# Optimization experiments

Hardware: AMD Instinct MI355X
Metric: run time of the kernel (lower is better)

The kernel has to match this reference:

```python
import jax, jax.numpy as jnp
import numpy as np

AABB0 = np.array([-1.5, -1.5, -1.5], np.float32)
AABB1 = np.array([1.5, 1.5, 1.5], np.float32)
GRID = (300, 300, 300)
NEAR, FAR = 2.0, 6.0
STEP = float(np.mean((AABB1 - AABB0) / (np.array(GRID, np.float32) - 1)) * 0.5)  # step_ratio=0.5
DIST_SCALE = 25.0
DENSITY_SHIFT = -10.0
W_THRES = 1e-4
PE = 2  # view_pe = feat_pe = 2
MAT = ((0, 1), (0, 2), (1, 2))
VEC = (2, 1, 0)
N_RAYS, N_SAMP = 1024, 512
DN, AN = 16, 16
APP_DIM, FEAT_C = 27, 128
IN_MLP = 2 * PE * 3 + 2 * PE * APP_DIM + 3 + APP_DIM  # 150


def posenc(x, freqs):
    fb = (2.0 ** jnp.arange(freqs)).astype(x.dtype)
    p = (x[..., None] * fb).reshape(x.shape[:-1] + (x.shape[-1] * freqs,))
    return jnp.concatenate([jnp.sin(p), jnp.cos(p)], -1)


def bilinear2d(plane, xy):
    # plane [C,H,W]; xy [P,2] in [-1,1], x->W, y->H; align_corners=True, border clamp
    C, H, W = plane.shape
    x = jnp.clip((xy[:, 0] * 0.5 + 0.5) * (W - 1), 0.0, W - 1)
    y = jnp.clip((xy[:, 1] * 0.5 + 0.5) * (H - 1), 0.0, H - 1)
    x0 = jnp.clip(jnp.floor(x), 0, W - 2).astype(jnp.int32)
    y0 = jnp.clip(jnp.floor(y), 0, H - 2).astype(jnp.int32)
    wx, wy = x - x0, y - y0
    v00 = plane[:, y0, x0]
    v01 = plane[:, y0, x0 + 1]
    v10 = plane[:, y0 + 1, x0]
    v11 = plane[:, y0 + 1, x0 + 1]
    return (v00 * (1 - wx) + v01 * wx) * (1 - wy) + (v10 * (1 - wx) + v11 * wx) * wy  # [C,P]


def linear1d(line, z):
    # line [C,L]; z [P] in [-1,1]
    C, L = line.shape
    t = jnp.clip((z * 0.5 + 0.5) * (L - 1), 0.0, L - 1)
    i0 = jnp.clip(jnp.floor(t), 0, L - 2).astype(jnp.int32)
    w = t - i0
    return line[:, i0] * (1 - w) + line[:, i0 + 1] * w  # [C,P]


def _forward(rays_o, rays_d, dplanes, dlines, aplanes, alines, basis_w,
             w1, b1, w2, b2, w3, b3, n_samples):
    a0, a1 = jnp.asarray(AABB0), jnp.asarray(AABB1)
    # --- sample_ray (is_train=False) ---
    vec = jnp.where(rays_d == 0, 1e-6, rays_d)
    rate_a = (a1 - rays_o) / vec
    rate_b = (a0 - rays_o) / vec
    t_min = jnp.clip(jnp.max(jnp.minimum(rate_a, rate_b), -1), NEAR, FAR)  # [R]
    rng = jnp.arange(n_samples, dtype=rays_o.dtype)[None]
    z_vals = t_min[:, None] + STEP * rng  # [R,S]
    pts = rays_o[:, None, :] + rays_d[:, None, :] * z_vals[..., None]  # [R,S,3]
    ray_valid = jnp.all((pts >= a0) & (pts <= a1), -1)  # [R,S]
    xn = ((pts - a0) * (2.0 / (a1 - a0)) - 1.0).reshape(-1, 3)  # normalize_coord -> [P,3]
    # --- density: VM decomposition (sum of plane*line products) ---
    sigma_feat = jnp.zeros((xn.shape[0],), xn.dtype)
    for i in range(3):
        p = bilinear2d(dplanes[i], xn[:, jnp.array(MAT[i])])
        l = linear1d(dlines[i], xn[:, VEC[i]])
        sigma_feat = sigma_feat + jnp.sum(p * l, 0)
    sigma = jax.nn.softplus(sigma_feat + DENSITY_SHIFT).reshape(z_vals.shape)
    sigma = jnp.where(ray_valid, sigma, 0.0)
    # --- raw2alpha compositing ---
    dists = jnp.concatenate([z_vals[:, 1:] - z_vals[:, :-1], jnp.zeros_like(z_vals[:, :1])], -1)
    alpha = 1.0 - jnp.exp(-sigma * dists * DIST_SCALE)
    T = jnp.cumprod(jnp.concatenate([jnp.ones_like(alpha[:, :1]), 1.0 - alpha + 1e-10], -1), -1)
    weight = alpha * T[:, :-1]
    app_mask = weight > W_THRES
    # --- appearance features + basis_mat ---
    coefs = [bilinear2d(aplanes[i], xn[:, jnp.array(MAT[i])]) * linear1d(alines[i], xn[:, VEC[i]])
             for i in range(3)]
    feat = jnp.concatenate(coefs, 0).T @ basis_w.T  # [P, app_dim]
    view = jnp.broadcast_to(rays_d[:, None, :], pts.shape).reshape(-1, 3)
    # --- MLPRender_Fea: [features, viewdirs, posenc(features), posenc(viewdirs)] ---
    mlp_in = jnp.concatenate([feat, view, posenc(feat, PE), posenc(view, PE)], -1)
    h = jax.nn.relu(mlp_in @ w1.T + b1)
    h = jax.nn.relu(h @ w2.T + b2)
    rgb = jax.nn.sigmoid(h @ w3.T + b3).reshape(z_vals.shape + (3,))
    rgb = jnp.where(app_mask[..., None], rgb, 0.0)
    acc = jnp.sum(weight, -1)
    rgb_map = jnp.sum(weight[..., None] * rgb, 1)
    rgb_map = jnp.clip(rgb_map + (1.0 - acc)[:, None], 0.0, 1.0)  # white background
    depth_map = jnp.sum(weight * z_vals, -1)
    return rgb_map, depth_map


def setup_inputs() -> dict:
    key = jax.random.key(0)
    ks = jax.random.split(key, 20)
    rd = jax.random.normal(ks[0], (N_RAYS, 3), jnp.float32)
    rays_d = rd / jnp.linalg.norm(rd, axis=-1, keepdims=True)
    rays_o = -3.0 * rays_d + 0.1 * jax.random.normal(ks[1], (N_RAYS, 3), jnp.float32)
    inp = {"rays_o": rays_o, "rays_d": rays_d}
    for i, ((m0, m1), v) in enumerate(zip(MAT, VEC)):
        inp[f"dplane{i}"] = jax.random.normal(ks[2 + i], (DN, GRID[m1], GRID[m0]), jnp.float32)
        inp[f"dline{i}"] = jax.random.normal(ks[5 + i], (DN, GRID[v]), jnp.float32)
        inp[f"aplane{i}"] = 0.1 * jax.random.normal(ks[8 + i], (AN, GRID[m1], GRID[m0]), jnp.float32)
        inp[f"aline{i}"] = 0.1 * jax.random.normal(ks[11 + i], (AN, GRID[v]), jnp.float32)
    inp["basis_w"] = 0.1 * jax.random.normal(ks[14], (APP_DIM, 3 * AN), jnp.float32)
    inp["w1"] = 0.05 * jax.random.normal(ks[15], (FEAT_C, IN_MLP), jnp.float32)
    inp["b1"] = jnp.zeros((FEAT_C,), jnp.float32)
    inp["w2"] = 0.05 * jax.random.normal(ks[16], (FEAT_C, FEAT_C), jnp.float32)
    inp["b2"] = jnp.zeros((FEAT_C,), jnp.float32)
    inp["w3"] = 0.05 * jax.random.normal(ks[17], (3, FEAT_C), jnp.float32)
    inp["b3"] = jnp.zeros((3,), jnp.float32)
    inp["n_samples"] = N_SAMP
    return inp


def reference(rays_o, rays_d, dplane0, dplane1, dplane2, dline0, dline1, dline2,
              aplane0, aplane1, aplane2, aline0, aline1, aline2, basis_w,
              w1, b1, w2, b2, w3, b3, n_samples):
    return _forward(rays_o, rays_d, (dplane0, dplane1, dplane2), (dline0, dline1, dline2),
                    (aplane0, aplane1, aplane2), (aline0, aline1, aline2), basis_w,
                    w1, b1, w2, b2, w3, b3, n_samples)
```

## Files before the change

kernel.cpp:

```cpp
#include <hip/hip_runtime.h>
#include <hip/hip_fp16.h>
#include <math.h>

#define NRAYS 1024
#define NSAMP 512
#define GRIDN 300
#define POS_ELEMS (GRIDN*GRIDN)
#define PLANE_ELEMS (16*POS_ELEMS)
#define CMAX 524288

typedef short bf16x8 __attribute__((ext_vector_type(8)));
typedef short short8 __attribute__((ext_vector_type(8)));
typedef float f32x4  __attribute__((ext_vector_type(4)));

struct H8v { __half2 h[4]; };

__device__ __forceinline__ float clampf(float x, float a, float b){ return fminf(fmaxf(x,a),b); }
__device__ __forceinline__ unsigned short f2b(float f){
    unsigned u = __builtin_bit_cast(unsigned, f);
    u = (u + 0x7FFFu + ((u>>16)&1u)) >> 16;
    return (unsigned short)u;
}
__device__ __forceinline__ float b2f(unsigned short h){
    unsigned u = ((unsigned)h) << 16;
    return __builtin_bit_cast(float, u);
}

__device__ __forceinline__ float ray_tmin(float o0,float o1,float o2,float d0,float d1,float d2){
    float v0=(d0==0.f)?1e-6f:d0, v1=(d1==0.f)?1e-6f:d1, v2=(d2==0.f)?1e-6f:d2;
    float t_min = -1e30f, a, b;
    a=(1.5f-o0)/v0; b=(-1.5f-o0)/v0; t_min=fmaxf(t_min,fminf(a,b));
    a=(1.5f-o1)/v1; b=(-1.5f-o1)/v1; t_min=fmaxf(t_min,fminf(a,b));
    a=(1.5f-o2)/v2; b=(-1.5f-o2)/v2; t_min=fmaxf(t_min,fminf(a,b));
    return clampf(t_min, 2.0f, 6.0f);
}

struct TPtrs {
    const float* psrc[6]; __half* pdst[6];
    const float* lsrc[6]; __half* ldst[6];
};

__global__ __launch_bounds__(256) void k_transpose(TPtrs tp) {
    int by  = blockIdx.y;
    int pos = blockIdx.x * 256 + threadIdx.x;
    if (pos < POS_ELEMS) {
        const float* src = tp.psrc[by];
        __half2 o[8];
        #pragma unroll
        for (int e = 0; e < 8; e++) {
            float a = src[(2*e  ) * POS_ELEMS + pos];
            float b = src[(2*e+1) * POS_ELEMS + pos];
            o[e] = __float22half2_rn(make_float2(a,b));
        }
        float4* dst = (float4*)(tp.pdst[by] + (size_t)pos * 16);
        dst[0] = *(float4*)&o[0];
        dst[1] = *(float4*)&o[4];
    }
    if (pos < GRIDN) {
        const float* ls = tp.lsrc[by];
        __half*      ld = tp.ldst[by];
        #pragma unroll
        for (int c = 0; c < 16; c++) ld[pos * 16 + c] = __float2half_rn(ls[c * GRIDN + pos]);
    }
}

__global__ __launch_bounds__(256) void k_prepw(
    const float* __restrict__ w1, const float* __restrict__ w2,
    unsigned short* __restrict__ w1b, unsigned short* __restrict__ w2b)
{
    int idx = blockIdx.x * 256 + threadIdx.x;
    if (idx < 128*160) {
        int j = idx / 160, k = idx - j*160;
        w1b[idx] = (k < 150) ? f2b(w1[j*150 + k]) : 0;
    } else if (idx < 128*160 + 128*128) {
        int i2 = idx - 128*160;
        w2b[i2] = f2b(w2[i2]);
    }
}

__global__ __launch_bounds__(256) void k_alpha(
    const float* __restrict__ ro, const float* __restrict__ rd,
    const __half* __restrict__ dpT0, const __half* __restrict__ dpT1, const __half* __restrict__ dpT2,
    const __half* __restrict__ dlT0, const __half* __restrict__ dlT1, const __half* __restrict__ dlT2,
    float* __restrict__ alpha_out)
{
    const float STEPF = (3.0f/299.0f)*0.5f;
    int gid = blockIdx.x*256 + threadIdx.x;
    int id = gid >> 1, h = gid & 1;
    int r = id >> 9, s = id & (NSAMP-1);

    float o0=ro[r*3+0], o1=ro[r*3+1], o2=ro[r*3+2];
    float d0=rd[r*3+0], d1=rd[r*3+1], d2=rd[r*3+2];
    float t_min = ray_tmin(o0,o1,o2,d0,d1,d2);

    float z  = t_min + STEPF * (float)s;
    float p0 = o0 + d0*z, p1 = o1 + d1*z, p2 = o2 + d2*z;
    bool valid = (p0>=-1.5f)&&(p0<=1.5f)&&(p1>=-1.5f)&&(p1<=1.5f)&&(p2>=-1.5f)&&(p2<=1.5f);

    float sfp = 0.f;
    if (valid) {
        float xn[3] = { (p0+1.5f)*(2.0f/3.0f)-1.0f,
                        (p1+1.5f)*(2.0f/3.0f)-1.0f,
                        (p2+1.5f)*(2.0f/3.0f)-1.0f };
        const __half* dpT[3] = {dpT0,dpT1,dpT2};
        const __half* dlT[3] = {dlT0,dlT1,dlT2};
        const int M0[3]={0,0,1}, M1[3]={1,2,2}, V[3]={2,1,0};
        #pragma unroll
        for (int i=0;i<3;i++) {
            float fx = clampf((xn[M0[i]]*0.5f+0.5f)*299.f, 0.f, 299.f);
            float fy = clampf((xn[M1[i]]*0.5f+0.5f)*299.f, 0.f, 299.f);
            float ft = clampf((xn[V[i]] *0.5f+0.5f)*299.f, 0.f, 299.f);
            int x0=min((int)fx,298), y0=min((int)fy,298), i0=min((int)ft,298);
            float wx=fx-(float)x0, wy=fy-(float)y0, wt=ft-(float)i0;
            __half2 w00=__float2half2_rn((1.f-wx)*(1.f-wy)), w01=__float2half2_rn(wx*(1.f-wy));
            __half2 w10=__float2half2_rn((1.f-wx)*wy),       w11=__float2half2_rn(wx*wy);
            __half2 u0 =__float2half2_rn(1.f-wt),            u1 =__float2half2_rn(wt);
            const __half* base = dpT[i] + (size_t)(y0*GRIDN+x0)*16 + h*8;
            H8v a00 = *(const H8v*)(base);
            H8v a01 = *(const H8v*)(base + 16);
            H8v a10 = *(const H8v*)(base + GRIDN*16);
            H8v a11 = *(const H8v*)(base + GRIDN*16 + 16);
            const __half* lb = dlT[i] + (size_t)i0*16 + h*8;
            H8v l0 = *(const H8v*)(lb);
            H8v l1 = *(const H8v*)(lb + 16);
            #pragma unroll
            for (int e=0;e<4;e++) {
                __half2 p = __hmul2(a00.h[e],w00);
                p = __hfma2(a01.h[e],w01,p);
                p = __hfma2(a10.h[e],w10,p);
                p = __hfma2(a11.h[e],w11,p);
                __half2 l = __hmul2(l0.h[e],u0);
                l = __hfma2(l1.h[e],u1,l);
                float2 c = __half22float2(__hmul2(p,l));
                sfp += c.x + c.y;
            }
        }
    }
    float sf = sfp + __shfl_xor(sfp, 1, 64);
    if (h == 0) {
        float sig = 0.f;
        if (valid) {
            float xs = sf - 10.0f;
            sig = fmaxf(xs, 0.f) + __logf(1.f + __expf(-fabsf(xs)));
        }
        alpha_out[id] = (s < NSAMP-1) ? (1.f - __expf(-sig * (STEPF*25.0f))) : 0.f;
    }
}

__global__ __launch_bounds__(256) void k_scan(
    const float* __restrict__ ro, const float* __restrict__ rd,
    const float* __restrict__ alpha_in,
    float* __restrict__ acc_out, float* __restrict__ depth_out,
    int* __restrict__ tmpl, float* __restrict__ tmpw, int* __restrict__ cnt)
{
    const float STEPF = (3.0f/299.0f)*0.5f;
    int r = blockIdx.x;
    int tid = threadIdx.x;
    int lane = tid & 63, wv = tid >> 6;

    float o0=ro[r*3+0], o1=ro[r*3+1], o2=ro[r*3+2];
    float d0=rd[r*3+0], d1=rd[r*3+1], d2=rd[r*3+2];
    float t_min = ray_tmin(o0,o1,o2,d0,d1,d2);

    float2 av = *(const float2*)&alpha_in[r*NSAMP + 2*tid];
    float aj0 = av.x, aj1 = av.y;
    float zj0 = t_min + STEPF * (float)(2*tid);
    float zj1 = t_min + STEPF * (float)(2*tid+1);

    float v0 = (1.f - aj0) + 1e-10f;
    float v1 = (1.f - aj1) + 1e-10f;
    float inc = v0 * v1;
    #pragma unroll
    for (int off=1; off<64; off<<=1) {
        float t = __shfl_up(inc, off, 64);
        if (lane >= off) inc *= t;
    }
    __shared__ float wtot[4], swsum[4], sdep[4];
    __shared__ int   wcnt[4];
    if (lane == 63) wtot[wv] = inc;
    __syncthreads();
    float pre = 1.f;
    for (int i=0;i<wv;i++) pre *= wtot[i];
    float excl = __shfl_up(inc, 1, 64);
    if (lane == 0) excl = 1.f;
    float T0 = pre * excl;
    float w0 = aj0 * T0;
    float w1 = aj1 * T0 * v0;

    float rw = w0 + w1, rz = w0*zj0 + w1*zj1;
    #pragma unroll
    for (int off=32; off>0; off>>=1) { rw += __shfl_xor(rw,off,64); rz += __shfl_xor(rz,off,64); }
    if (lane == 0) { swsum[wv] = rw; sdep[wv] = rz; }

    bool act0 = (w0 > 1e-4f), act1 = (w1 > 1e-4f);
    unsigned long long m0 = __ballot(act0);
    unsigned long long m1 = __ballot(act1);
    int tot = __popcll(m0) + __popcll(m1);
    if (lane == 0) wcnt[wv] = tot;
    __syncthreads();
    int base = 0;
    for (int i=0;i<wv;i++) base += wcnt[i];
    unsigned long long below = (1ull<<lane)-1ull;
    int o = base + __popcll(m0 & below) + __popcll(m1 & below);
    int* tl = tmpl + r*NSAMP;
    float* tw = tmpw + r*NSAMP;
    if (act0) { tl[o] = (r<<9)|(2*tid);   tw[o] = w0; o++; }
    if (act1) { tl[o] = (r<<9)|(2*tid+1); tw[o] = w1; }

    if (tid == 0) {
        float a=0.f, b=0.f;
        #pragma unroll
        for (int i=0;i<4;i++){ a+=swsum[i]; b+=sdep[i]; }
        acc_out[r] = a; depth_out[r] = b;
        cnt[r] = wcnt[0]+wcnt[1]+wcnt[2]+wcnt[3];
    }
}

__global__ __launch_bounds__(256) void k_compact(
    const int* __restrict__ tmpl, const float* __restrict__ tmpw,
    const int* __restrict__ cnt,
    int* __restrict__ basep, int* __restrict__ counter,
    int* __restrict__ list, float* __restrict__ wlist)
{
    int r = blockIdx.x;
    int tid = threadIdx.x, lane = tid & 63, wv = tid >> 6;

    int accb = 0, acct = 0;
    for (int i = tid; i < NRAYS; i += 256) {
        int c = cnt[i];
        acct += c;
        if (i < r) accb += c;
    }
    #pragma unroll
    for (int off=32; off>0; off>>=1) {
        accb += __shfl_xor(accb, off, 64);
        acct += __shfl_xor(acct, off, 64);
    }
    __shared__ int sb[4], st[4];
    if (lane == 0) { sb[wv] = accb; st[wv] = acct; }
    __syncthreads();
    int b = sb[0]+sb[1]+sb[2]+sb[3];
    int n = cnt[r];
    if (tid == 0) {
        basep[r] = b;
        if (r == 0) *counter = st[0]+st[1]+st[2]+st[3];
    }
    const int* tl = tmpl + r*NSAMP;
    const float* tw = tmpw + r*NSAMP;
    for (int j = tid; j < n; j += 256) {
        list[b+j]  = tl[j];
        wlist[b+j] = tw[j];
    }
}

__global__ __launch_bounds__(256) void k_gather(
    const float* __restrict__ ro, const float* __restrict__ rd,
    const __half* __restrict__ apT0, const __half* __restrict__ apT1, const __half* __restrict__ apT2,
    const __half* __restrict__ alT0, const __half* __restrict__ alT1, const __half* __restrict__ alT2,
    const float* __restrict__ basis_w,
    const int* __restrict__ list, const int* __restrict__ counter,
    float* __restrict__ Xf)
{
    const float STEPF = (3.0f/299.0f)*0.5f;
    int gid = blockIdx.x*256 + threadIdx.x;
    int idx = gid >> 3, q = gid & 7;
    int count = *counter;
    if (idx >= count) return;

    int sid = list[idx];
    int r = sid >> 9, s = sid & (NSAMP-1);
    float o0=ro[r*3+0], o1=ro[r*3+1], o2=ro[r*3+2];
    float d0=rd[r*3+0], d1=rd[r*3+1], d2=rd[r*3+2];
    float t_min = ray_tmin(o0,o1,o2,d0,d1,d2);
    float z = t_min + STEPF*(float)s;
    float xn[3] = { ((o0+d0*z)+1.5f)*(2.0f/3.0f)-1.0f,
                    ((o1+d1*z)+1.5f)*(2.0f/3.0f)-1.0f,
                    ((o2+d2*z)+1.5f)*(2.0f/3.0f)-1.0f };

    bool active = (q < 6);
    int i = min(q >> 1, 2);
    int h = q & 1;

    float c8[8];
    {
        const __half* apT[3]={apT0,apT1,apT2};
        const __half* alT[3]={alT0,alT1,alT2};
        const int M0[3]={0,0,1}, M1[3]={1,2,2}, V[3]={2,1,0};
        float fx = clampf((xn[M0[i]]*0.5f+0.5f)*299.f, 0.f, 299.f);
        float fy = clampf((xn[M1[i]]*0.5f+0.5f)*299.f, 0.f, 299.f);
        float ft = clampf((xn[V[i]] *0.5f+0.5f)*299.f, 0.f, 299.f);
        int x0=min((int)fx,298), y0=min((int)fy,298), i0=min((int)ft,298);
        float wx=fx-(float)x0, wy=fy-(float)y0, wt=ft-(float)i0;
        __half2 w00=__float2half2_rn((1.f-wx)*(1.f-wy)), w01=__float2half2_rn(wx*(1.f-wy));
        __half2 w10=__float2half2_rn((1.f-wx)*wy),       w11=__float2half2_rn(wx*wy);
        __half2 u0 =__float2half2_rn(1.f-wt),            u1 =__float2half2_rn(wt);
        if (active) {
            const __half* base = apT[i] + (size_t)(y0*GRIDN+x0)*16 + h*8;
            H8v a00 = *(const H8v*)(base);
            H8v a01 = *(const H8v*)(base + 16);
            H8v a10 = *(const H8v*)(base + GRIDN*16);
            H8v a11 = *(const H8v*)(base + GRIDN*16 + 16);
            const __half* lb = alT[i] + (size_t)i0*16 + h*8;
            H8v l0 = *(const H8v*)(lb);
            H8v l1 = *(const H8v*)(lb + 16);
            #pragma unroll
            for (int e=0;e<4;e++) {
                __half2 p = __hmul2(a00.h[e],w00);
                p = __hfma2(a01.h[e],w01,p);
                p = __hfma2(a10.h[e],w10,p);
                p = __hfma2(a11.h[e],w11,p);
                __half2 l = __hmul2(l0.h[e],u0);
                l = __hfma2(l1.h[e],u1,l);
                float2 c = __half22float2(__hmul2(p,l));
                c8[2*e]   = c.x;
                c8[2*e+1] = c.y;
            }
        } else {
            #pragma unroll
            for (int e=0;e<8;e++) c8[e] = 0.f;
        }
    }

    float kv[4] = {0.f, 0.f, 0.f, 0.f};
    #pragma unroll
    for (int j=0;j<27;j++) {
        const float4* b4 = (const float4*)(basis_w + j*48 + i*16 + h*8);
        float4 b0 = b4[0], b1 = b4[1];
        float p = b0.x*c8[0] + b0.y*c8[1] + b0.z*c8[2] + b0.w*c8[3]
                + b1.x*c8[4] + b1.y*c8[5] + b1.z*c8[6] + b1.w*c8[7];
        p += __shfl_xor(p, 1, 64);
        p += __shfl_xor(p, 2, 64);
        p += __shfl_xor(p, 4, 64);
        if (q == (j >> 2)) kv[j & 3] = p;
    }

    float4 v = make_float4(kv[0], kv[1], kv[2], kv[3]);
    if (q == 6) v.w = d0;
    if (q == 7) { v = make_float4(d1, d2, 0.f, 0.f); }
    *(float4*)&Xf[(size_t)idx*32 + q*4] = v;
}

#define XST 168
#define HST 136
#define TIL 32
#define XFS 36

__global__ __launch_bounds__(512, 4) void k_gemm(
    const float* __restrict__ Xf,
    const unsigned short* __restrict__ w1b, const float* __restrict__ b1p,
    const unsigned short* __restrict__ w2b, const float* __restrict__ b2p,
    const float* __restrict__ w3p, const float* __restrict__ b3p,
    const float* __restrict__ wlist, const int* __restrict__ counter,
    __half* __restrict__ contrib)
{
    __shared__ __align__(16) unsigned short Xs[TIL*XST];
    __shared__ __align__(16) unsigned short Hs[TIL*HST];
    __shared__ __align__(16) float Xf_s[2][TIL][XFS];

    int tid  = threadIdx.x;
    int wvid = tid >> 6, lane = tid & 63, ln15 = lane & 15, kq = lane >> 4;

    int count  = *counter;
    int ntiles = (count + TIL-1) >> 5;
    if ((int)blockIdx.x >= ntiles) return;

    int jrow = (wvid<<4) + ln15;
    bf16x8 w1f[5], w2f[4];
    #pragma unroll
    for (int ks=0; ks<5; ks++)
        w1f[ks] = *(const bf16x8*)&w1b[jrow*160 + ks*32 + kq*8];
    #pragma unroll
    for (int ks=0; ks<4; ks++)
        w2f[ks] = *(const bf16x8*)&w2b[jrow*128 + ks*32 + kq*8];
    float bias1 = b1p[jrow];
    float bias2 = b2p[jrow];

    int srow = tid >> 3, sq = tid & 7;

    int cur = 0;
    {
        if (tid < TIL*8) {
            int idx = blockIdx.x*TIL + srow;
            float4 v = make_float4(0.f,0.f,0.f,0.f);
            if (idx < count) v = *(const float4*)&Xf[(size_t)idx*32 + sq*4];
            *(float4*)&Xf_s[0][srow][sq*4] = v;
        }
        __syncthreads();
    }

    for (int t = blockIdx.x; t < ntiles; t += gridDim.x) {
        int tn = t + gridDim.x;
        bool havepf = (tn < ntiles) && (tid < TIL*8);
        float4 pf = make_float4(0.f,0.f,0.f,0.f);
        if (havepf) {
            int idx = tn*TIL + srow;
            if (idx < count) pf = *(const float4*)&Xf[(size_t)idx*32 + sq*4];
        }

        for (int u = tid; u < TIL*30; u += 512) {
            int row = u / 30, j = u - row*30;
            unsigned short* X = &Xs[row*XST];
            float f = Xf_s[cur][row][j];
            float s1 = __sinf(f), s2 = __sinf(2.f*f);
            float c1 = __cosf(f), c2 = __cosf(2.f*f);
            int c = j - 27;
            int o_s = (j < 27) ? (30 + 2*j) : (138 + 2*c);
            int o_c = (j < 27) ? (84 + 2*j) : (144 + 2*c);
            X[o_s]   = f2b(s1); X[o_s+1] = f2b(s2);
            X[o_c]   = f2b(c1); X[o_c+1] = f2b(c2);
            if ((j & 1) == 0) {
                float fB = Xf_s[cur][row][j+1];
                unsigned pk = (unsigned)f2b(f) | ((unsigned)f2b(fB) << 16);
                *(unsigned*)&X[j] = pk;
            }
        }
        for (int u = tid; u < TIL*10; u += 512) {
            int row = u / 10, k = 150 + (u - row*10);
            Xs[row*XST + k] = 0;
        }
        __syncthreads();

        {
            f32x4 acc[2] = {};
            #pragma unroll
            for (int ks=0; ks<5; ks++) {
                int ko = ks*32 + kq*8;
                #pragma unroll
                for (int m=0;m<2;m++) {
                    bf16x8 a = *(const bf16x8*)&Xs[(m*16 + ln15)*XST + ko];
                    acc[m] = __builtin_amdgcn_mfma_f32_16x16x32_bf16(a, w1f[ks], acc[m], 0,0,0);
                }
            }
            int col = jrow;
            #pragma unroll
            for (int m=0;m<2;m++) {
                int rbase = m*16 + kq*4;
                #pragma unroll
                for (int j=0;j<4;j++)
                    Hs[(rbase+j)*HST + col] = f2b(fmaxf(acc[m][j] + bias1, 0.f));
            }
        }
        __syncthreads();

        {
            f32x4 acc[2] = {};
            #pragma unroll
            for (int ks=0; ks<4; ks++) {
                int ko = ks*32 + kq*8;
                #pragma unroll
                for (int m=0;m<2;m++) {
                    bf16x8 a = *(const bf16x8*)&Hs[(m*16 + ln15)*HST + ko];
                    acc[m] = __builtin_amdgcn_mfma_f32_16x16x32_bf16(a, w2f[ks], acc[m], 0,0,0);
                }
            }
            int col = jrow;
            #pragma unroll
            for (int m=0;m<2;m++) {
                int rbase = m*16 + kq*4;
                #pragma unroll
                for (int j=0;j<4;j++)
                    Xs[(rbase+j)*HST + col] = f2b(fmaxf(acc[m][j] + bias2, 0.f));
            }
        }
        __syncthreads();

        if (havepf)
            *(float4*)&Xf_s[cur^1][srow][sq*4] = pf;

        if (tid < TIL*8) {
            int u = tid >> 3, q = tid & 7;
            int idx = t*TIL + u;
            if (q < 6 && idx < count) {
                int ch = q >> 1, hf = q & 1;
                float wgt = wlist[idx];
                const unsigned short* h2 = Xs + u*HST + hf*64;
                const float* wr = w3p + ch*128 + hf*64;
                float pa[4] = {0.f, 0.f, 0.f, 0.f};
                #pragma unroll
                for (int kc=0;kc<8;kc++) {
                    bf16x8 hv = *(const bf16x8*)&h2[kc*8];
                    const float* wrk = wr + kc*8;
                    float tacc = 0.f;
                    #pragma unroll
                    for (int e=0;e<8;e++)
                        tacc += b2f((unsigned short)hv[e]) * wrk[e];
                    pa[kc & 3] += tacc;
                }
                float p = (pa[0] + pa[1]) + (pa[2] + pa[3]);
                p += __shfl_xor(p, 1, 64);
                if (hf == 0) {
                    float v = 0.f;
                    if (wgt > 0.f) {
                        float acc5 = b3p[ch] + p;
                        v = wgt * (1.f/(1.f + __expf(-acc5)));
                    }
                    contrib[(size_t)ch*CMAX + idx] = __float2half(v);
                }
            }
        }
        __syncthreads();
        cur ^= 1;
    }
}

__global__ __launch_bounds__(128) void k_rgbsum(
    const __half* __restrict__ contrib,
    const int* __restrict__ cnt, const int* __restrict__ basep,
    const float* __restrict__ acc_out, float* __restrict__ out)
{
    int r = blockIdx.x;
    int n = cnt[r], b = basep[r];
    int tid = threadIdx.x, lane = tid & 63, w = tid >> 6;
    float s0=0.f, s1=0.f, s2=0.f;
    for (int j = tid; j < n; j += 128) {
        s0 += __half2float(contrib[0*CMAX + b + j]);
        s1 += __half2float(contrib[1*CMAX + b + j]);
        s2 += __half2float(contrib[2*CMAX + b + j]);
    }
    #pragma unroll
    for (int off=32; off>0; off>>=1) {
        s0 += __shfl_xor(s0,off,64); s1 += __shfl_xor(s1,off,64); s2 += __shfl_xor(s2,off,64);
    }
    __shared__ float sh[3][2];
    if (lane == 0) { sh[0][w]=s0; sh[1][w]=s1; sh[2][w]=s2; }
    __syncthreads();
    if (tid == 0) {
        float bg = 1.f - acc_out[r];
        out[r*3+0] = clampf(sh[0][0]+sh[0][1] + bg, 0.f, 1.f);
        out[r*3+1] = clampf(sh[1][0]+sh[1][1] + bg, 0.f, 1.f);
        out[r*3+2] = clampf(sh[2][0]+sh[2][1] + bg, 0.f, 1.f);
    }
}

extern "C" void kernel_launch(void* const* d_in, const int* in_sizes, int n_in,
                              void* d_out, int out_size, void* d_ws, size_t ws_size,
                              hipStream_t stream)
{
    const float* ro = (const float*)d_in[0];
    const float* rd = (const float*)d_in[1];
    const float* dplane[3] = {(const float*)d_in[2],(const float*)d_in[6],(const float*)d_in[10]};
    const float* dline[3]  = {(const float*)d_in[3],(const float*)d_in[7],(const float*)d_in[11]};
    const float* aplane[3] = {(const float*)d_in[4],(const float*)d_in[8],(const float*)d_in[12]};
    const float* aline[3]  = {(const float*)d_in[5],(const float*)d_in[9],(const float*)d_in[13]};
    const float* basis_w = (const float*)d_in[14];
    const float* w1 = (const float*)d_in[15];
    const float* b1 = (const float*)d_in[16];
    const float* w2 = (const float*)d_in[17];
    const float* b2 = (const float*)d_in[18];
    const float* w3 = (const float*)d_in[19];
    const float* b3 = (const float*)d_in[20];
    float* out = (float*)d_out;

    char* ws = (char*)d_ws;
    int*    counter  = (int*)   (ws + 0);
    float*  accb     = (float*) (ws + 12544);
    float*  wlist    = (float*) (ws + 16640);
    int*    list     = (int*)   (ws + 2113792);
    __half* planesT  = (__half*)(ws + 4210944);
    __half* linesT   = (__half*)(ws + 21490944);
    unsigned short* w1b = (unsigned short*)(ws + 21548544);
    unsigned short* w2b = (unsigned short*)(ws + 21589504);
    float*  alphab   = (float*) (ws + 21622272);
    int*    cntb     = (int*)   (ws + 23719424);
    int*    baseb    = (int*)   (ws + 23723520);
    int*    tmpl     = (int*)   (ws + 23727616);
    float*  tmpw     = (float*) (ws + 25824768);
    __half* contrib  = (__half*)(ws + 23727616);
    float*  Xf       = (float*) (ws + 27921920);


    TPtrs tp;
    for (int i=0;i<3;i++) {
        tp.psrc[i]   = dplane[i]; tp.pdst[i]   = planesT + (size_t)i*PLANE_ELEMS;
        tp.psrc[3+i] = aplane[i]; tp.pdst[3+i] = planesT + (size_t)(3+i)*PLANE_ELEMS;
        tp.lsrc[i]   = dline[i];  tp.ldst[i]   = linesT + i*(GRIDN*16);
        tp.lsrc[3+i] = aline[i];  tp.ldst[3+i] = linesT + (3+i)*(GRIDN*16);
    }
    dim3 tg((POS_ELEMS+255)/256, 6);
    hipLaunchKernelGGL(k_transpose, tg, dim3(256), 0, stream, tp);

    k_prepw<<<(128*160 + 128*128 + 255)/256, 256, 0, stream>>>(w1, w2, w1b, w2b);

    k_alpha<<<(NRAYS*NSAMP*2)/256, 256, 0, stream>>>(
        ro, rd,
        planesT + 0*(size_t)PLANE_ELEMS, planesT + 1*(size_t)PLANE_ELEMS, planesT + 2*(size_t)PLANE_ELEMS,
        linesT + 0*(GRIDN*16), linesT + 1*(GRIDN*16), linesT + 2*(GRIDN*16),
        alphab);

    k_scan<<<NRAYS, 256, 0, stream>>>(
        ro, rd, alphab, accb, out + NRAYS*3, tmpl, tmpw, cntb);

    k_compact<<<NRAYS, 256, 0, stream>>>(tmpl, tmpw, cntb, baseb, counter, list, wlist);

    k_gather<<<(CMAX*8)/256, 256, 0, stream>>>(
        ro, rd,
        planesT + 3*(size_t)PLANE_ELEMS, planesT + 4*(size_t)PLANE_ELEMS, planesT + 5*(size_t)PLANE_ELEMS,
        linesT + 3*(GRIDN*16), linesT + 4*(GRIDN*16), linesT + 5*(GRIDN*16),
        basis_w, list, counter, Xf);

    k_gemm<<<512, 512, 0, stream>>>(
        Xf, w1b, b1, w2b, b2, w3, b3,
        wlist, counter, contrib);

    k_rgbsum<<<NRAYS, 128, 0, stream>>>(contrib, cntb, baseb, accb, out);
}
```

Measured before the change: 96.47 us.

## Fuse alpha and scan kernels, merge weight prep into transpose, grid-stride gather

Fuses the density/alpha kernel and the per-ray transmittance scan into one 1024-thread block per ray, so alpha values stay in shared memory instead of making a global round-trip. The bf16 weight conversion becomes an extra blockIdx.y slice of the transpose kernel, which removes one launch. The gather kernel switches to a grid-stride loop over a fixed 4096-block grid rather than launching for the worst-case count. The costs are three extra block-wide syncs in which 768 of the 1024 threads sit idle during the scan, and lower occupancy from the larger blocks.

```diff
diff --git a/kernel.cpp b/kernel.cpp
--- a/kernel.cpp
+++ b/kernel.cpp
@@ -40,8 +40,22 @@
     const float* lsrc[6]; __half* ldst[6];
 };
 
-__global__ __launch_bounds__(256) void k_transpose(TPtrs tp) {
+__global__ __launch_bounds__(256) void k_transpose(TPtrs tp,
+    const float* __restrict__ w1, const float* __restrict__ w2,
+    unsigned short* __restrict__ w1b, unsigned short* __restrict__ w2b)
+{
     int by  = blockIdx.y;
+    if (by == 6) {
+        int idx = blockIdx.x * 256 + threadIdx.x;
+        if (idx < 128*160) {
+            int j = idx / 160, k = idx - j*160;
+            w1b[idx] = (k < 150) ? f2b(w1[j*150 + k]) : 0;
+        } else if (idx < 128*160 + 128*128) {
+            int i2 = idx - 128*160;
+            w2b[i2] = f2b(w2[i2]);
+        }
+        return;
+    }
     int pos = blockIdx.x * 256 + threadIdx.x;
     if (pos < POS_ELEMS) {
         const float* src = tp.psrc[by];
@@ -64,155 +78,142 @@
     }
 }
 
-__global__ __launch_bounds__(256) void k_prepw(
-    const float* __restrict__ w1, const float* __restrict__ w2,
-    unsigned short* __restrict__ w1b, unsigned short* __restrict__ w2b)
-{
-    int idx = blockIdx.x * 256 + threadIdx.x;
-    if (idx < 128*160) {
-        int j = idx / 160, k = idx - j*160;
-        w1b[idx] = (k < 150) ? f2b(w1[j*150 + k]) : 0;
-    } else if (idx < 128*160 + 128*128) {
-        int i2 = idx - 128*160;
-        w2b[i2] = f2b(w2[i2]);
-    }
-}
-
-__global__ __launch_bounds__(256) void k_alpha(
+__global__ __launch_bounds__(1024) void k_alphascan(
     const float* __restrict__ ro, const float* __restrict__ rd,
     const __half* __restrict__ dpT0, const __half* __restrict__ dpT1, const __half* __restrict__ dpT2,
     const __half* __restrict__ dlT0, const __half* __restrict__ dlT1, const __half* __restrict__ dlT2,
-    float* __restrict__ alpha_out)
-{
-    const float STEPF = (3.0f/299.0f)*0.5f;
-    int gid = blockIdx.x*256 + threadIdx.x;
-    int id = gid >> 1, h = gid & 1;
-    int r = id >> 9, s = id & (NSAMP-1);
-
-    float o0=ro[r*3+0], o1=ro[r*3+1], o2=ro[r*3+2];
-    float d0=rd[r*3+0], d1=rd[r*3+1], d2=rd[r*3+2];
-    float t_min = ray_tmin(o0,o1,o2,d0,d1,d2);
-
-    float z  = t_min + STEPF * (float)s;
-    float p0 = o0 + d0*z, p1 = o1 + d1*z, p2 = o2 + d2*z;
-    bool valid = (p0>=-1.5f)&&(p0<=1.5f)&&(p1>=-1.5f)&&(p1<=1.5f)&&(p2>=-1.5f)&&(p2<=1.5f);
-
-    float sfp = 0.f;
-    if (valid) {
-        float xn[3] = { (p0+1.5f)*(2.0f/3.0f)-1.0f,
-                        (p1+1.5f)*(2.0f/3.0f)-1.0f,
-                        (p2+1.5f)*(2.0f/3.0f)-1.0f };
-        const __half* dpT[3] = {dpT0,dpT1,dpT2};
-        const __half* dlT[3] = {dlT0,dlT1,dlT2};
-        const int M0[3]={0,0,1}, M1[3]={1,2,2}, V[3]={2,1,0};
-        #pragma unroll
-        for (int i=0;i<3;i++) {
-            float fx = clampf((xn[M0[i]]*0.5f+0.5f)*299.f, 0.f, 299.f);
-            float fy = clampf((xn[M1[i]]*0.5f+0.5f)*299.f, 0.f, 299.f);
-            float ft = clampf((xn[V[i]] *0.5f+0.5f)*299.f, 0.f, 299.f);
-            int x0=min((int)fx,298), y0=min((int)fy,298), i0=min((int)ft,298);
-            float wx=fx-(float)x0, wy=fy-(float)y0, wt=ft-(float)i0;
-            __half2 w00=__float2half2_rn((1.f-wx)*(1.f-wy)), w01=__float2half2_rn(wx*(1.f-wy));
-            __half2 w10=__float2half2_rn((1.f-wx)*wy),       w11=__float2half2_rn(wx*wy);
-            __half2 u0 =__float2half2_rn(1.f-wt),            u1 =__float2half2_rn(wt);
-            const __half* base = dpT[i] + (size_t)(y0*GRIDN+x0)*16 + h*8;
-            H8v a00 = *(const H8v*)(base);
-            H8v a01 = *(const H8v*)(base + 16);
-            H8v a10 = *(const H8v*)(base + GRIDN*16);
-            H8v a11 = *(const H8v*)(base + GRIDN*16 + 16);
-            const __half* lb = dlT[i] + (size_t)i0*16 + h*8;
-            H8v l0 = *(const H8v*)(lb);
-            H8v l1 = *(const H8v*)(lb + 16);
-            #pragma unroll
-            for (int e=0;e<4;e++) {
-                __half2 p = __hmul2(a00.h[e],w00);
-                p = __hfma2(a01.h[e],w01,p);
-                p = __hfma2(a10.h[e],w10,p);
-                p = __hfma2(a11.h[e],w11,p);
-                __half2 l = __hmul2(l0.h[e],u0);
-                l = __hfma2(l1.h[e],u1,l);
-                float2 c = __half22float2(__hmul2(p,l));
-                sfp += c.x + c.y;
-            }
-        }
-    }
-    float sf = sfp + __shfl_xor(sfp, 1, 64);
-    if (h == 0) {
-        float sig = 0.f;
-        if (valid) {
-            float xs = sf - 10.0f;
-            sig = fmaxf(xs, 0.f) + __logf(1.f + __expf(-fabsf(xs)));
-        }
-        alpha_out[id] = (s < NSAMP-1) ? (1.f - __expf(-sig * (STEPF*25.0f))) : 0.f;
-    }
-}
-
-__global__ __launch_bounds__(256) void k_scan(
-    const float* __restrict__ ro, const float* __restrict__ rd,
-    const float* __restrict__ alpha_in,
     float* __restrict__ acc_out, float* __restrict__ depth_out,
     int* __restrict__ tmpl, float* __restrict__ tmpw, int* __restrict__ cnt)
 {
     const float STEPF = (3.0f/299.0f)*0.5f;
     int r = blockIdx.x;
     int tid = threadIdx.x;
-    int lane = tid & 63, wv = tid >> 6;
+    int s = tid >> 1, h = tid & 1;
+
+    __shared__ float alpha_s[NSAMP];
+    __shared__ float wtot[4], swsum[4], sdep[4];
+    __shared__ int   wcnt[4];
 
     float o0=ro[r*3+0], o1=ro[r*3+1], o2=ro[r*3+2];
     float d0=rd[r*3+0], d1=rd[r*3+1], d2=rd[r*3+2];
     float t_min = ray_tmin(o0,o1,o2,d0,d1,d2);
 
-    float2 av = *(const float2*)&alpha_in[r*NSAMP + 2*tid];
-    float aj0 = av.x, aj1 = av.y;
-    float zj0 = t_min + STEPF * (float)(2*tid);
-    float zj1 = t_min + STEPF * (float)(2*tid+1);
-
-    float v0 = (1.f - aj0) + 1e-10f;
-    float v1 = (1.f - aj1) + 1e-10f;
-    float inc = v0 * v1;
-    #pragma unroll
-    for (int off=1; off<64; off<<=1) {
-        float t = __shfl_up(inc, off, 64);
-        if (lane >= off) inc *= t;
-    }
-    __shared__ float wtot[4], swsum[4], sdep[4];
-    __shared__ int   wcnt[4];
-    if (lane == 63) wtot[wv] = inc;
+    {
+        float z  = t_min + STEPF * (float)s;
+        float p0 = o0 + d0*z, p1 = o1 + d1*z, p2 = o2 + d2*z;
+        bool valid = (p0>=-1.5f)&&(p0<=1.5f)&&(p1>=-1.5f)&&(p1<=1.5f)&&(p2>=-1.5f)&&(p2<=1.5f);
+
+        float sfp = 0.f;
+        if (valid) {
+            float xn[3] = { (p0+1.5f)*(2.0f/3.0f)-1.0f,
+                            (p1+1.5f)*(2.0f/3.0f)-1.0f,
+                            (p2+1.5f)*(2.0f/3.0f)-1.0f };
+            const __half* dpT[3] = {dpT0,dpT1,dpT2};
+            const __half* dlT[3] = {dlT0,dlT1,dlT2};
+            const int M0[3]={0,0,1}, M1[3]={1,2,2}, V[3]={2,1,0};
+            #pragma unroll
+            for (int i=0;i<3;i++) {
+                float fx = clampf((xn[M0[i]]*0.5f+0.5f)*299.f, 0.f, 299.f);
+                float fy = clampf((xn[M1[i]]*0.5f+0.5f)*299.f, 0.f, 299.f);
+                float ft = clampf((xn[V[i]] *0.5f+0.5f)*299.f, 0.f, 299.f);
+                int x0=min((int)fx,298), y0=min((int)fy,298), i0=min((int)ft,298);
+                float wx=fx-(float)x0, wy=fy-(float)y0, wt=ft-(float)i0;
+                __half2 w00=__float2half2_rn((1.f-wx)*(1.f-wy)), w01=__float2half2_rn(wx*(1.f-wy));
+                __half2 w10=__float2half2_rn((1.f-wx)*wy),       w11=__float2half2_rn(wx*wy);
+                __half2 u0 =__float2half2_rn(1.f-wt),            u1 =__float2half2_rn(wt);
+                const __half* base = dpT[i] + (size_t)(y0*GRIDN+x0)*16 + h*8;
+                H8v a00 = *(const H8v*)(base);
+                H8v a01 = *(const H8v*)(base + 16);
+                H8v a10 = *(const H8v*)(base + GRIDN*16);
+                H8v a11 = *(const H8v*)(base + GRIDN*16 + 16);
+                const __half* lb = dlT[i] + (size_t)i0*16 + h*8;
+                H8v l0 = *(const H8v*)(lb);
+                H8v l1 = *(const H8v*)(lb + 16);
+                #pragma unroll
+                for (int e=0;e<4;e++) {
+                    __half2 p = __hmul2(a00.h[e],w00);
+                    p = __hfma2(a01.h[e],w01,p);
+                    p = __hfma2(a10.h[e],w10,p);
+                    p = __hfma2(a11.h[e],w11,p);
+                    __half2 l = __hmul2(l0.h[e],u0);
+                    l = __hfma2(l1.h[e],u1,l);
+                    float2 c = __half22float2(__hmul2(p,l));
+                    sfp += c.x + c.y;
+                }
+            }
+        }
+        float sf = sfp + __shfl_xor(sfp, 1, 64);
+        if (h == 0) {
+            float sig = 0.f;
+            if (valid) {
+                float xs = sf - 10.0f;
+                sig = fmaxf(xs, 0.f) + __logf(1.f + __expf(-fabsf(xs)));
+            }
+            alpha_s[s] = (s < NSAMP-1) ? (1.f - __expf(-sig * (STEPF*25.0f))) : 0.f;
+        }
+    }
     __syncthreads();
-    float pre = 1.f;
-    for (int i=0;i<wv;i++) pre *= wtot[i];
-    float excl = __shfl_up(inc, 1, 64);
-    if (lane == 0) excl = 1.f;
-    float T0 = pre * excl;
-    float w0 = aj0 * T0;
-    float w1 = aj1 * T0 * v0;
-
-    float rw = w0 + w1, rz = w0*zj0 + w1*zj1;
-    #pragma unroll
-    for (int off=32; off>0; off>>=1) { rw += __shfl_xor(rw,off,64); rz += __shfl_xor(rz,off,64); }
-    if (lane == 0) { swsum[wv] = rw; sdep[wv] = rz; }
-
-    bool act0 = (w0 > 1e-4f), act1 = (w1 > 1e-4f);
-    unsigned long long m0 = __ballot(act0);
-    unsigned long long m1 = __ballot(act1);
-    int tot = __popcll(m0) + __popcll(m1);
-    if (lane == 0) wcnt[wv] = tot;
+
+    int lane = tid & 63, wv = tid >> 6;
+    float aj0=0.f, aj1=0.f, zj0=0.f, zj1=0.f, inc=1.f, v0=1.f, v1=1.f;
+    if (tid < 256) {
+        aj0 = alpha_s[2*tid]; aj1 = alpha_s[2*tid+1];
+        zj0 = t_min + STEPF * (float)(2*tid);
+        zj1 = t_min + STEPF * (float)(2*tid+1);
+        v0 = (1.f - aj0) + 1e-10f;
+        v1 = (1.f - aj1) + 1e-10f;
+        inc = v0 * v1;
+        #pragma unroll
+        for (int off=1; off<64; off<<=1) {
+            float t = __shfl_up(inc, off, 64);
+            if (lane >= off) inc *= t;
+        }
+        if (lane == 63) wtot[wv] = inc;
+    }
     __syncthreads();
-    int base = 0;
-    for (int i=0;i<wv;i++) base += wcnt[i];
-    unsigned long long below = (1ull<<lane)-1ull;
-    int o = base + __popcll(m0 & below) + __popcll(m1 & below);
-    int* tl = tmpl + r*NSAMP;
-    float* tw = tmpw + r*NSAMP;
-    if (act0) { tl[o] = (r<<9)|(2*tid);   tw[o] = w0; o++; }
-    if (act1) { tl[o] = (r<<9)|(2*tid+1); tw[o] = w1; }
-
-    if (tid == 0) {
-        float a=0.f, b=0.f;
+
+    float w0=0.f, w1=0.f;
+    unsigned long long m0=0, m1=0;
+    bool act0=false, act1=false;
+    if (tid < 256) {
+        float pre = 1.f;
+        for (int i=0;i<wv;i++) pre *= wtot[i];
+        float excl = __shfl_up(inc, 1, 64);
+        if (lane == 0) excl = 1.f;
+        float T0 = pre * excl;
+        w0 = aj0 * T0;
+        w1 = aj1 * T0 * v0;
+
+        float rw = w0 + w1, rz = w0*zj0 + w1*zj1;
         #pragma unroll
-        for (int i=0;i<4;i++){ a+=swsum[i]; b+=sdep[i]; }
-        acc_out[r] = a; depth_out[r] = b;
-        cnt[r] = wcnt[0]+wcnt[1]+wcnt[2]+wcnt[3];
+        for (int off=32; off>0; off>>=1) { rw += __shfl_xor(rw,off,64); rz += __shfl_xor(rz,off,64); }
+        if (lane == 0) { swsum[wv] = rw; sdep[wv] = rz; }
+
+        act0 = (w0 > 1e-4f); act1 = (w1 > 1e-4f);
+        m0 = __ballot(act0);
+        m1 = __ballot(act1);
+        int tot = __popcll(m0) + __popcll(m1);
+        if (lane == 0) wcnt[wv] = tot;
+    }
+    __syncthreads();
+
+    if (tid < 256) {
+        int base = 0;
+        for (int i=0;i<wv;i++) base += wcnt[i];
+        unsigned long long below = (1ull<<lane)-1ull;
+        int o = base + __popcll(m0 & below) + __popcll(m1 & below);
+        int* tl = tmpl + r*NSAMP;
+        float* tw = tmpw + r*NSAMP;
+        if (act0) { tl[o] = (r<<9)|(2*tid);   tw[o] = w0; o++; }
+        if (act1) { tl[o] = (r<<9)|(2*tid+1); tw[o] = w1; }
+
+        if (tid == 0) {
+            float a=0.f, b=0.f;
+            #pragma unroll
+            for (int i=0;i<4;i++){ a+=swsum[i]; b+=sdep[i]; }
+            acc_out[r] = a; depth_out[r] = b;
+            cnt[r] = wcnt[0]+wcnt[1]+wcnt[2]+wcnt[3];
+        }
     }
 }
 
@@ -262,10 +263,10 @@
     float* __restrict__ Xf)
 {
     const float STEPF = (3.0f/299.0f)*0.5f;
-    int gid = blockIdx.x*256 + threadIdx.x;
-    int idx = gid >> 3, q = gid & 7;
     int count = *counter;
-    if (idx >= count) return;
+    int total = count * 8;
+    for (int u = blockIdx.x*256 + threadIdx.x; u < total; u += gridDim.x*256) {
+    int idx = u >> 3, q = u & 7;
 
     int sid = list[idx];
     int r = sid >> 9, s = sid & (NSAMP-1);
@@ -338,6 +339,7 @@
     if (q == 6) v.w = d0;
     if (q == 7) { v = make_float4(d1, d2, 0.f, 0.f); }
     *(float4*)&Xf[(size_t)idx*32 + q*4] = v;
+    }
 }
 
 #define XST 168
@@ -560,7 +562,6 @@
     __half* linesT   = (__half*)(ws + 21490944);
     unsigned short* w1b = (unsigned short*)(ws + 21548544);
     unsigned short* w2b = (unsigned short*)(ws + 21589504);
-    float*  alphab   = (float*) (ws + 21622272);
     int*    cntb     = (int*)   (ws + 23719424);
     int*    baseb    = (int*)   (ws + 23723520);
     int*    tmpl     = (int*)   (ws + 23727616);
@@ -576,23 +577,18 @@
         tp.lsrc[i]   = dline[i];  tp.ldst[i]   = linesT + i*(GRIDN*16);
         tp.lsrc[3+i] = aline[i];  tp.ldst[3+i] = linesT + (3+i)*(GRIDN*16);
     }
-    dim3 tg((POS_ELEMS+255)/256, 6);
-    hipLaunchKernelGGL(k_transpose, tg, dim3(256), 0, stream, tp);
-
-    k_prepw<<<(128*160 + 128*128 + 255)/256, 256, 0, stream>>>(w1, w2, w1b, w2b);
-
-    k_alpha<<<(NRAYS*NSAMP*2)/256, 256, 0, stream>>>(
+    dim3 tg((POS_ELEMS+255)/256, 7);
+    hipLaunchKernelGGL(k_transpose, tg, dim3(256), 0, stream, tp, w1, w2, w1b, w2b);
+
+    k_alphascan<<<NRAYS, 1024, 0, stream>>>(
         ro, rd,
         planesT + 0*(size_t)PLANE_ELEMS, planesT + 1*(size_t)PLANE_ELEMS, planesT + 2*(size_t)PLANE_ELEMS,
         linesT + 0*(GRIDN*16), linesT + 1*(GRIDN*16), linesT + 2*(GRIDN*16),
-        alphab);
-
-    k_scan<<<NRAYS, 256, 0, stream>>>(
-        ro, rd, alphab, accb, out + NRAYS*3, tmpl, tmpw, cntb);
+        accb, out + NRAYS*3, tmpl, tmpw, cntb);
 
     k_compact<<<NRAYS, 256, 0, stream>>>(tmpl, tmpw, cntb, baseb, counter, list, wlist);
 
-    k_gather<<<(CMAX*8)/256, 256, 0, stream>>>(
+    k_gather<<<4096, 256, 0, stream>>>(
         ro, rd,
         planesT + 3*(size_t)PLANE_ELEMS, planesT + 4*(size_t)PLANE_ELEMS, planesT + 5*(size_t)PLANE_ELEMS,
         linesT + 3*(GRIDN*16), linesT + 4*(GRIDN*16), linesT + 5*(GRIDN*16),
```

Measured after the change: 146.7 us. +52.0%, slower.
